# Optimization experiments

Measured on AMD Instinct MI355X. Metric: run time of the kernel, lower is better.

The kernel has to match this reference:

```python
import jax, jax.numpy as jnp
import numpy as np

DIM = 512
HEADS = 8
DIM_HEAD = 64
HIDDEN = HEADS * DIM_HEAD
SCALE = DIM_HEAD ** -0.5


def rmsnorm_ch(x, g):
    # F.normalize over channel dim (axis=1), then * g * sqrt(C)
    # x: [b, c, l], g: [c]
    n = jnp.maximum(jnp.linalg.norm(x, axis=1, keepdims=True), 1e-12)
    c = x.shape[1]
    return (x / n) * g[None, :, None] * (c ** 0.5)


def setup_inputs() -> dict:
    key = jax.random.key(0)
    ks = jax.random.split(key, 6)
    b, l = 8, 4096
    x = jax.random.normal(ks[0], (b, DIM, l), dtype=jnp.float32)
    g_in = jnp.ones((DIM,), dtype=jnp.float32)
    # conv1d kernel_size=1 == matmul; kaiming-ish init scale
    w_qkv = jax.random.normal(ks[1], (3 * HIDDEN, DIM), dtype=jnp.float32) * (1.0 / np.sqrt(DIM))
    w_out = jax.random.normal(ks[2], (DIM, HIDDEN), dtype=jnp.float32) * (1.0 / np.sqrt(HIDDEN))
    b_out = jax.random.normal(ks[3], (DIM,), dtype=jnp.float32) * 0.01
    g_out = jnp.ones((DIM,), dtype=jnp.float32)
    return {"x": x, "g_in": g_in, "w_qkv": w_qkv, "w_out": w_out, "b_out": b_out, "g_out": g_out}


def reference(x, g_in, w_qkv, w_out, b_out, g_out):
    b, c, l = x.shape
    residual = x
    xn = rmsnorm_ch(x, g_in)                       # [b, c, l]
    qkv = jnp.einsum('oc,bcl->bol', w_qkv, xn)     # [b, 3*hidden, l]
    q, k, v = jnp.split(qkv, 3, axis=1)            # each [b, hidden, l]
    def to_heads(t):
        return t.reshape(b, HEADS, DIM_HEAD, l)    # [b, h, d, l]
    q, k, v = to_heads(q), to_heads(k), to_heads(v)
    q = jax.nn.softmax(q, axis=2) * SCALE          # softmax over head-dim d
    k = jax.nn.softmax(k, axis=3)                  # softmax over sequence l
    context = jnp.einsum('bhdn,bhen->bhde', k, v)  # [b, h, d, e]
    out = jnp.einsum('bhde,bhdn->bhen', context, q)  # [b, h, e, l]
    out = out.reshape(b, HIDDEN, l)
    o = jnp.einsum('ch,bhl->bcl', w_out, out) + b_out[None, :, None]
    o = rmsnorm_ch(o, g_out)
    return o + residual
```

## Files before the change

### kernel.cpp

```cpp
#include <hip/hip_runtime.h>


#define BB 8
#define CC 512
#define LL 4096
#define HH 8
#define DH 64
#define TC 1536

__device__ __constant__ const float SQRT_C = 22.62741699796952f;
#define SCALE_Q 0.125f

typedef unsigned short bfr_t;
typedef __attribute__((ext_vector_type(8))) short short8;
typedef __attribute__((ext_vector_type(4))) float f32x4;

__device__ __forceinline__ float bf2f(bfr_t v) {
  union { unsigned u; float f; } c; c.u = ((unsigned)v) << 16; return c.f;
}
__device__ __forceinline__ bfr_t f2bf(float f) {
  union { float f; unsigned u; } c; c.f = f;
  unsigned u = c.u + 0x7fffu + ((c.u >> 16) & 1u);
  return (bfr_t)(u >> 16);
}

__device__ __forceinline__ void load_lds16(const bfr_t* g, short* l) {
  __builtin_amdgcn_global_load_lds(
      (const __attribute__((address_space(1))) void*)g,
      (__attribute__((address_space(3))) void*)l, 16, 0, 0);
}

__global__ __launch_bounds__(256) void conv_bf16(const float* __restrict__ in,
                                                 bfr_t* __restrict__ out, int n) {
  int i = blockIdx.x * 256 + threadIdx.x;
  if (i < n) out[i] = f2bf(in[i]);
}

__global__ __launch_bounds__(256) void fused_norm_transpose(
    const float* __restrict__ x, const float* __restrict__ g,
    bfr_t* __restrict__ xt) {
  __shared__ float tile[64][65];
  __shared__ float red[4][64];
  __shared__ float invn_s[64];
  int b = blockIdx.y, l0 = blockIdx.x * 64;
  int t = threadIdx.x, ll = t & 63, cg = t >> 6;
  const float* xb = x + (size_t)b * CC * LL + l0;
  float vals[8][16];
  float ss = 0.f;
#pragma unroll
  for (int ch = 0; ch < 8; ++ch) {
    int c0 = ch * 64;
#pragma unroll
    for (int i = 0; i < 16; ++i) {
      int c = i * 4 + cg;
      float v = xb[(size_t)(c0 + c) * LL + ll];
      vals[ch][i] = v;
      ss += v * v;
    }
  }
  red[cg][ll] = ss;
  __syncthreads();
  if (cg == 0) {
    float s = red[0][ll] + red[1][ll] + red[2][ll] + red[3][ll];
    invn_s[ll] = SQRT_C / fmaxf(sqrtf(s), 1e-12f);
  }
  __syncthreads();
  int lw = t >> 2, ccw = (t & 3) * 16;
  float iv = invn_s[lw];
#pragma unroll
  for (int ch = 0; ch < 8; ++ch) {
    int c0 = ch * 64;
#pragma unroll
    for (int i = 0; i < 16; ++i) tile[i * 4 + cg][ll] = vals[ch][i];
    __syncthreads();
    union { short s[16]; f32x4 v[2]; } pk;
#pragma unroll
    for (int u = 0; u < 16; ++u) {
      int c = ccw + u;
      pk.s[u] = (short)f2bf(tile[c][lw] * g[c0 + c] * iv);
    }
    bfr_t* dst = xt + ((size_t)b * LL + l0 + lw) * CC + c0 + ccw;
    *(f32x4*)dst = pk.v[0];
    *(f32x4*)(dst + 8) = pk.v[1];
    __syncthreads();
  }
}

__global__ __launch_bounds__(256) void gemm_bf16(
    const bfr_t* __restrict__ A, const bfr_t* __restrict__ Bt,
    bfr_t* __restrict__ Cout, const float* __restrict__ bias, int M) {
  const int K = 512;
  __shared__ short As[128 * 64];
  __shared__ short Bs[128 * 64];
  int b = blockIdx.z;
  int m0 = blockIdx.y * 128, n0 = blockIdx.x * 128;
  int t = threadIdx.x, lane = t & 63, wid = t >> 6;
  int wm = wid & 1, wn = wid >> 1;
  int quad = lane >> 4, r = lane & 15, r7 = r & 7;
  const bfr_t* Bbase = Bt + (size_t)b * LL * K;

  int lrow = lane >> 3;
  int lgran = (lane & 7) ^ lrow;
  const bfr_t* gA[4];
  const bfr_t* gB[4];
  short* lA[4];
  short* lB[4];
#pragma unroll
  for (int u = 0; u < 4; ++u) {
    int ch = wid * 4 + u;
    int row = ch * 8 + lrow;
    gA[u] = A + (size_t)(m0 + row) * K + lgran * 8;
    gB[u] = Bbase + (size_t)(n0 + row) * K + lgran * 8;
    lA[u] = As + ch * 512;
    lB[u] = Bs + ch * 512;
  }

  f32x4 acc[4][4] = {};

  for (int k0 = 0; k0 < K; k0 += 64) {
    __syncthreads();
#pragma unroll
    for (int u = 0; u < 4; ++u) {
      load_lds16(gA[u] + k0, lA[u]);
      load_lds16(gB[u] + k0, lB[u]);
    }
    __syncthreads();
#pragma unroll
    for (int ks = 0; ks < 2; ++ks) {
      short8 af[4], bfr8[4];
#pragma unroll
      for (int i = 0; i < 4; ++i) {
        int ga = ((ks * 4 + quad) ^ r7) * 8;
        af[i]   = *(const short8*)&As[(wm * 64 + i * 16 + r) * 64 + ga];
        bfr8[i] = *(const short8*)&Bs[(wn * 64 + i * 16 + r) * 64 + ga];
      }
#pragma unroll
      for (int i = 0; i < 4; ++i)
#pragma unroll
        for (int j = 0; j < 4; ++j)
          acc[i][j] = __builtin_amdgcn_mfma_f32_16x16x32_bf16(af[i], bfr8[j],
                                                              acc[i][j], 0, 0, 0);
    }
  }

  bfr_t* Cb = Cout + (size_t)b * M * LL;
#pragma unroll
  for (int i = 0; i < 4; ++i) {
#pragma unroll
    for (int reg = 0; reg < 4; ++reg) {
      int row = m0 + wm * 64 + i * 16 + quad * 4 + reg;
      float bi = bias ? bias[row] : 0.f;
#pragma unroll
      for (int j = 0; j < 4; ++j) {
        int col = n0 + wn * 64 + j * 16 + r;
        Cb[(size_t)row * LL + col] = f2bf(acc[i][j][reg] + bi);
      }
    }
  }
}

__global__ __launch_bounds__(256) void kstats(const bfr_t* __restrict__ qkv,
                                              float* __restrict__ kmax,
                                              float* __restrict__ ksum) {
  __shared__ float red[256];
  int row = blockIdx.x;
  int b = row >> 9, hd = row & 511;
  const bfr_t* kr = qkv + ((size_t)b * TC + 512 + hd) * LL;
  int t = threadIdx.x;
  float vals[16];
  float m = -1e30f;
#pragma unroll
  for (int i = 0; i < 16; ++i) {
    float v = bf2f(kr[t + i * 256]);
    vals[i] = v;
    m = fmaxf(m, v);
  }
  red[t] = m;
  __syncthreads();
  for (int s = 128; s > 0; s >>= 1) {
    if (t < s) red[t] = fmaxf(red[t], red[t + s]);
    __syncthreads();
  }
  m = red[0];
  __syncthreads();
  float ss = 0.f;
#pragma unroll
  for (int i = 0; i < 16; ++i) ss += __expf(vals[i] - m);
  red[t] = ss;
  __syncthreads();
  for (int s = 128; s > 0; s >>= 1) {
    if (t < s) red[t] += red[t + s];
    __syncthreads();
  }
  if (t == 0) { kmax[row] = m; ksum[row] = red[0]; }
}

__global__ __launch_bounds__(256) void context_mfma(
    const bfr_t* __restrict__ qkv, const float* __restrict__ kmax,
    float* __restrict__ ctx_p) {
  __shared__ float red[4][4096];
  int s = blockIdx.x, bh = blockIdx.y;
  int b = bh >> 3, h = bh & 7;
  int t = threadIdx.x, lane = t & 63, wid = t >> 6;
  int quad = lane >> 4, r = lane & 15;
  const bfr_t* kb = qkv + ((size_t)b * TC + 512 + h * 64) * LL;
  const bfr_t* vb = qkv + ((size_t)b * TC + 1024 + h * 64) * LL;
  float km[4];
#pragma unroll
  for (int i = 0; i < 4; ++i) km[i] = kmax[b * 512 + h * 64 + i * 16 + r];
  int n_base = s * 512 + wid * 128;
  f32x4 acc[4][4] = {};
#pragma unroll
  for (int ks = 0; ks < 4; ++ks) {
    int n0 = n_base + ks * 32;
    short8 af[4], bf8[4];
#pragma unroll
    for (int i = 0; i < 4; ++i) {
      union { short s[8]; short8 v8; } uk;
      uk.v8 = *(const short8*)&kb[(size_t)(i * 16 + r) * LL + n0 + quad * 8];
#pragma unroll
      for (int jj = 0; jj < 8; ++jj)
        uk.s[jj] = (short)f2bf(__expf(bf2f((bfr_t)uk.s[jj]) - km[i]));
      af[i] = uk.v8;
      bf8[i] = *(const short8*)&vb[(size_t)(i * 16 + r) * LL + n0 + quad * 8];
    }
#pragma unroll
    for (int i = 0; i < 4; ++i)
#pragma unroll
      for (int j = 0; j < 4; ++j)
        acc[i][j] = __builtin_amdgcn_mfma_f32_16x16x32_bf16(af[i], bf8[j],
                                                            acc[i][j], 0, 0, 0);
  }
#pragma unroll
  for (int i = 0; i < 4; ++i)
#pragma unroll
    for (int j = 0; j < 4; ++j)
#pragma unroll
      for (int reg = 0; reg < 4; ++reg)
        red[wid][(i * 16 + quad * 4 + reg) * 64 + j * 16 + r] = acc[i][j][reg];
  __syncthreads();
  float* out = ctx_p + ((size_t)bh * 8 + s) * 4096;
#pragma unroll
  for (int u = 0; u < 16; ++u) {
    int idx = u * 256 + t;
    out[idx] = red[0][idx] + red[1][idx] + red[2][idx] + red[3][idx];
  }
}

__global__ __launch_bounds__(256) void context_reduce(
    const float* __restrict__ ctx_p, const float* __restrict__ ksum,
    bfr_t* __restrict__ ctx_bf) {
  int bh = blockIdx.x;
  int b = bh >> 3, h = bh & 7;
  int t = threadIdx.x;
#pragma unroll
  for (int i = 0; i < 16; ++i) {
    int idx = i * 256 + t;
    int d = idx >> 6;
    float sum = 0.f;
#pragma unroll
    for (int s = 0; s < 8; ++s) sum += ctx_p[((size_t)bh * 8 + s) * 4096 + idx];
    ctx_bf[(size_t)bh * 4096 + idx] = f2bf(sum / ksum[b * 512 + h * 64 + d]);
  }
}

__global__ __launch_bounds__(256) void apply_fused(
    const bfr_t* __restrict__ qkv, const bfr_t* __restrict__ ctx_bf,
    bfr_t* __restrict__ out_t) {
  int b = blockIdx.z, h = blockIdx.y;
  int t = threadIdx.x, lane = t & 63, wid = t >> 6;
  int quad = lane >> 4, r = lane & 15;
  int n0 = blockIdx.x * 256 + wid * 64;
  const bfr_t* qb = qkv + ((size_t)b * TC + h * 64) * LL;
  const bfr_t* cb = ctx_bf + (size_t)(b * HH + h) * 4096;
  float v[4][16];
  float pm[4];
#pragma unroll
  for (int i = 0; i < 4; ++i) {
    pm[i] = -1e30f;
#pragma unroll
    for (int ks = 0; ks < 2; ++ks)
#pragma unroll
      for (int jj = 0; jj < 8; ++jj) {
        float q = bf2f(qb[(size_t)(ks * 32 + quad * 8 + jj) * LL + n0 + i * 16 + r]);
        v[i][ks * 8 + jj] = q;
        pm[i] = fmaxf(pm[i], q);
      }
  }
#pragma unroll
  for (int i = 0; i < 4; ++i) {
    pm[i] = fmaxf(pm[i], __shfl_xor(pm[i], 16, 64));
    pm[i] = fmaxf(pm[i], __shfl_xor(pm[i], 32, 64));
  }
  float psum[4];
#pragma unroll
  for (int i = 0; i < 4; ++i) {
    float s = 0.f;
#pragma unroll
    for (int u = 0; u < 16; ++u) { v[i][u] = __expf(v[i][u] - pm[i]); s += v[i][u]; }
    psum[i] = s;
  }
#pragma unroll
  for (int i = 0; i < 4; ++i) {
    psum[i] += __shfl_xor(psum[i], 16, 64);
    psum[i] += __shfl_xor(psum[i], 32, 64);
  }
  short8 af[2][4];
#pragma unroll
  for (int i = 0; i < 4; ++i) {
    float sc = SCALE_Q / psum[i];
#pragma unroll
    for (int ks = 0; ks < 2; ++ks) {
      union { short s[8]; short8 v8; } u;
#pragma unroll
      for (int jj = 0; jj < 8; ++jj) u.s[jj] = (short)f2bf(v[i][ks * 8 + jj] * sc);
      af[ks][i] = u.v8;
    }
  }
  short8 bfrag[2][4];
#pragma unroll
  for (int ks = 0; ks < 2; ++ks)
#pragma unroll
    for (int j = 0; j < 4; ++j) {
      union { short s[8]; short8 v8; } u;
#pragma unroll
      for (int jj = 0; jj < 8; ++jj)
        u.s[jj] = (short)cb[(ks * 32 + quad * 8 + jj) * 64 + j * 16 + r];
      bfrag[ks][j] = u.v8;
    }
  f32x4 acc[4][4] = {};
#pragma unroll
  for (int ks = 0; ks < 2; ++ks)
#pragma unroll
    for (int i = 0; i < 4; ++i)
#pragma unroll
      for (int j = 0; j < 4; ++j)
        acc[i][j] = __builtin_amdgcn_mfma_f32_16x16x32_bf16(af[ks][i], bfrag[ks][j],
                                                            acc[i][j], 0, 0, 0);
  bfr_t* dst = out_t + (size_t)b * LL * 512 + h * 64;
#pragma unroll
  for (int i = 0; i < 4; ++i)
#pragma unroll
    for (int reg = 0; reg < 4; ++reg) {
      int row = n0 + i * 16 + quad * 4 + reg;
#pragma unroll
      for (int j = 0; j < 4; ++j)
        dst[(size_t)row * 512 + j * 16 + r] = f2bf(acc[i][j][reg]);
    }
}

__global__ __launch_bounds__(256) void final_norm_res(
    const bfr_t* __restrict__ o, const float* __restrict__ g,
    const float* __restrict__ x, float* __restrict__ out) {
  __shared__ float red[4][64];
  __shared__ float invn[64];
  int b = blockIdx.y, l0 = blockIdx.x * 64;
  int t = threadIdx.x, ll = t & 63, cg = t >> 6;
  const bfr_t* ob = o + (size_t)b * CC * LL + l0 + ll;
  float ss = 0.f;
  for (int c = cg * 128; c < cg * 128 + 128; ++c) {
    float v = bf2f(ob[(size_t)c * LL]);
    ss += v * v;
  }
  red[cg][ll] = ss;
  __syncthreads();
  if (cg == 0) {
    float s = red[0][ll] + red[1][ll] + red[2][ll] + red[3][ll];
    invn[ll] = SQRT_C / fmaxf(sqrtf(s), 1e-12f);
  }
  __syncthreads();
  float iv = invn[ll];
  const float* xb = x + (size_t)b * CC * LL + l0 + ll;
  float* outb = out + (size_t)b * CC * LL + l0 + ll;
  for (int c = cg * 128; c < cg * 128 + 128; ++c) {
    float v = bf2f(ob[(size_t)c * LL]);
    outb[(size_t)c * LL] = v * g[c] * iv + xb[(size_t)c * LL];
  }
}

extern "C" void kernel_launch(void* const* d_in, const int* in_sizes, int n_in,
                              void* d_out, int out_size, void* d_ws,
                              size_t ws_size, hipStream_t stream) {
  const float* x     = (const float*)d_in[0];
  const float* g_in  = (const float*)d_in[1];
  const float* w_qkv = (const float*)d_in[2];
  const float* w_out = (const float*)d_in[3];
  const float* b_out = (const float*)d_in[4];
  const float* g_out = (const float*)d_in[5];
  float* out = (float*)d_out;

  char* ws = (char*)d_ws;
  const size_t off_wqkv  = 0;
  const size_t off_wout  = 1572864;
  const size_t off_kmax  = 2097152;
  const size_t off_ksum  = 2244608;
  const size_t off_ctx   = 2260992;
  const size_t off_ctxp  = 3309568;
  const size_t off_xt    = 11698176;
  const size_t off_qkv   = 45252608;
  const size_t ws_need   = 145915904;
  if (ws_size < ws_need) return;

  bfr_t* wqkv_bf = (bfr_t*)(ws + off_wqkv);
  bfr_t* wout_bf = (bfr_t*)(ws + off_wout);
  float* kmax    = (float*)(ws + off_kmax);
  float* ksum    = (float*)(ws + off_ksum);
  bfr_t* ctx_bf  = (bfr_t*)(ws + off_ctx);
  float* ctxp    = (float*)(ws + off_ctxp);
  bfr_t* xt      = (bfr_t*)(ws + off_xt);
  bfr_t* qkv     = (bfr_t*)(ws + off_qkv);
  bfr_t* o_bf    = (bfr_t*)(ws + off_qkv);

  conv_bf16<<<dim3((1536 * 512 + 255) / 256), 256, 0, stream>>>(w_qkv, wqkv_bf, 1536 * 512);
  conv_bf16<<<dim3((512 * 512 + 255) / 256), 256, 0, stream>>>(w_out, wout_bf, 512 * 512);
  fused_norm_transpose<<<dim3(LL / 64, BB), 256, 0, stream>>>(x, g_in, xt);
  gemm_bf16<<<dim3(LL / 128, TC / 128, BB), 256, 0, stream>>>(wqkv_bf, xt, qkv, nullptr, TC);
  kstats<<<dim3(BB * 512), 256, 0, stream>>>(qkv, kmax, ksum);
  context_mfma<<<dim3(8, BB * HH), 256, 0, stream>>>(qkv, kmax, ctxp);
  context_reduce<<<dim3(BB * HH), 256, 0, stream>>>(ctxp, ksum, ctx_bf);
  apply_fused<<<dim3(LL / 256, HH, BB), 256, 0, stream>>>(qkv, ctx_bf, xt);
  gemm_bf16<<<dim3(LL / 128, CC / 128, BB), 256, 0, stream>>>(wout_bf, xt, o_bf, b_out, CC);
  final_norm_res<<<dim3(LL / 64, BB), 256, 0, stream>>>(o_bf, g_out, x, out);
}
```

Before: 310.7 us.

## Switch GEMM to 32x32 MFMA, vectorize kstats loads, widen final norm, merge weight casts

The bf16 GEMM now uses 32x32x16 MFMA tiles with 2x2 accumulators per wave instead of 16x16x32 with 4x4, which cuts the number of LDS fragment reads and MFMA issues. kstats now reads each thread's 16 contiguous bf16 values with two 16-byte loads instead of strided scalar loads. final_norm_res runs 512 threads, caches its values in registers and reads the intermediate only once. The two weight conversion kernels are merged into a single launch. Risks are higher register pressure from the 64-value array in final_norm_res and a changed LDS bank pattern in the swizzled fragment reads.

```diff
diff --git a/kernel.cpp b/kernel.cpp
--- a/kernel.cpp
+++ b/kernel.cpp
@@ -14,6 +14,7 @@
 typedef unsigned short bfr_t;
 typedef __attribute__((ext_vector_type(8))) short short8;
 typedef __attribute__((ext_vector_type(4))) float f32x4;
+typedef __attribute__((ext_vector_type(16))) float f32x16;
 
 __device__ __forceinline__ float bf2f(bfr_t v) {
   union { unsigned u; float f; } c; c.u = ((unsigned)v) << 16; return c.f;
@@ -30,10 +31,13 @@
       (__attribute__((address_space(3))) void*)l, 16, 0, 0);
 }
 
-__global__ __launch_bounds__(256) void conv_bf16(const float* __restrict__ in,
-                                                 bfr_t* __restrict__ out, int n) {
+__global__ __launch_bounds__(256) void conv_bf16_2(
+    const float* __restrict__ in1, bfr_t* __restrict__ o1, int n1,
+    const float* __restrict__ in2, bfr_t* __restrict__ o2, int n2) {
   int i = blockIdx.x * 256 + threadIdx.x;
-  if (i < n) out[i] = f2bf(in[i]);
+  if (i < n1) o1[i] = f2bf(in1[i]);
+  int j = i - n1;
+  if (j >= 0 && j < n2) o2[j] = f2bf(in2[j]);
 }
 
 __global__ __launch_bounds__(256) void fused_norm_transpose(
@@ -96,7 +100,7 @@
   int m0 = blockIdx.y * 128, n0 = blockIdx.x * 128;
   int t = threadIdx.x, lane = t & 63, wid = t >> 6;
   int wm = wid & 1, wn = wid >> 1;
-  int quad = lane >> 4, r = lane & 15, r7 = r & 7;
+  int l31 = lane & 31, half = lane >> 5;
   const bfr_t* Bbase = Bt + (size_t)b * LL * K;
 
   int lrow = lane >> 3;
@@ -115,7 +119,7 @@
     lB[u] = Bs + ch * 512;
   }
 
-  f32x4 acc[4][4] = {};
+  f32x16 acc[2][2] = {};
 
   for (int k0 = 0; k0 < K; k0 += 64) {
     __syncthreads();
@@ -126,34 +130,40 @@
     }
     __syncthreads();
 #pragma unroll
-    for (int ks = 0; ks < 2; ++ks) {
-      short8 af[4], bfr8[4];
-#pragma unroll
-      for (int i = 0; i < 4; ++i) {
-        int ga = ((ks * 4 + quad) ^ r7) * 8;
-        af[i]   = *(const short8*)&As[(wm * 64 + i * 16 + r) * 64 + ga];
-        bfr8[i] = *(const short8*)&Bs[(wn * 64 + i * 16 + r) * 64 + ga];
+    for (int kk = 0; kk < 4; ++kk) {
+      short8 a[2], bq[2];
+#pragma unroll
+      for (int im = 0; im < 2; ++im) {
+        int row = wm * 64 + im * 32 + l31;
+        int gk = (kk * 2 + half) ^ (row & 7);
+        a[im] = *(const short8*)&As[row * 64 + gk * 8];
       }
 #pragma unroll
-      for (int i = 0; i < 4; ++i)
-#pragma unroll
-        for (int j = 0; j < 4; ++j)
-          acc[i][j] = __builtin_amdgcn_mfma_f32_16x16x32_bf16(af[i], bfr8[j],
-                                                              acc[i][j], 0, 0, 0);
+      for (int jn = 0; jn < 2; ++jn) {
+        int row = wn * 64 + jn * 32 + l31;
+        int gk = (kk * 2 + half) ^ (row & 7);
+        bq[jn] = *(const short8*)&Bs[row * 64 + gk * 8];
+      }
+#pragma unroll
+      for (int im = 0; im < 2; ++im)
+#pragma unroll
+        for (int jn = 0; jn < 2; ++jn)
+          acc[im][jn] = __builtin_amdgcn_mfma_f32_32x32x16_bf16(
+              a[im], bq[jn], acc[im][jn], 0, 0, 0);
     }
   }
 
   bfr_t* Cb = Cout + (size_t)b * M * LL;
 #pragma unroll
-  for (int i = 0; i < 4; ++i) {
-#pragma unroll
-    for (int reg = 0; reg < 4; ++reg) {
-      int row = m0 + wm * 64 + i * 16 + quad * 4 + reg;
+  for (int im = 0; im < 2; ++im) {
+#pragma unroll
+    for (int reg = 0; reg < 16; ++reg) {
+      int row = m0 + wm * 64 + im * 32 + (reg & 3) + 8 * (reg >> 2) + 4 * half;
       float bi = bias ? bias[row] : 0.f;
 #pragma unroll
-      for (int j = 0; j < 4; ++j) {
-        int col = n0 + wn * 64 + j * 16 + r;
-        Cb[(size_t)row * LL + col] = f2bf(acc[i][j][reg] + bi);
+      for (int jn = 0; jn < 2; ++jn) {
+        int col = n0 + wn * 64 + jn * 32 + l31;
+        Cb[(size_t)row * LL + col] = f2bf(acc[im][jn][reg] + bi);
       }
     }
   }
@@ -165,13 +175,16 @@
   __shared__ float red[256];
   int row = blockIdx.x;
   int b = row >> 9, hd = row & 511;
-  const bfr_t* kr = qkv + ((size_t)b * TC + 512 + hd) * LL;
+  const bfr_t* kr = qkv + ((size_t)b * TC + 512 + hd) * LL + (size_t)threadIdx.x * 16;
   int t = threadIdx.x;
+  union { short s[16]; short8 v[2]; } u;
+  u.v[0] = *(const short8*)kr;
+  u.v[1] = *(const short8*)(kr + 8);
   float vals[16];
   float m = -1e30f;
 #pragma unroll
   for (int i = 0; i < 16; ++i) {
-    float v = bf2f(kr[t + i * 256]);
+    float v = bf2f((bfr_t)u.s[i]);
     vals[i] = v;
     m = fmaxf(m, v);
   }
@@ -349,32 +362,39 @@
     }
 }
 
-__global__ __launch_bounds__(256) void final_norm_res(
+__global__ __launch_bounds__(512) void final_norm_res(
     const bfr_t* __restrict__ o, const float* __restrict__ g,
     const float* __restrict__ x, float* __restrict__ out) {
-  __shared__ float red[4][64];
+  __shared__ float red[8][64];
   __shared__ float invn[64];
   int b = blockIdx.y, l0 = blockIdx.x * 64;
   int t = threadIdx.x, ll = t & 63, cg = t >> 6;
   const bfr_t* ob = o + (size_t)b * CC * LL + l0 + ll;
+  float vals[64];
   float ss = 0.f;
-  for (int c = cg * 128; c < cg * 128 + 128; ++c) {
+#pragma unroll
+  for (int i = 0; i < 64; ++i) {
+    int c = cg * 64 + i;
     float v = bf2f(ob[(size_t)c * LL]);
+    vals[i] = v;
     ss += v * v;
   }
   red[cg][ll] = ss;
   __syncthreads();
   if (cg == 0) {
-    float s = red[0][ll] + red[1][ll] + red[2][ll] + red[3][ll];
+    float s = 0.f;
+#pragma unroll
+    for (int j = 0; j < 8; ++j) s += red[j][ll];
     invn[ll] = SQRT_C / fmaxf(sqrtf(s), 1e-12f);
   }
   __syncthreads();
   float iv = invn[ll];
   const float* xb = x + (size_t)b * CC * LL + l0 + ll;
   float* outb = out + (size_t)b * CC * LL + l0 + ll;
-  for (int c = cg * 128; c < cg * 128 + 128; ++c) {
-    float v = bf2f(ob[(size_t)c * LL]);
-    outb[(size_t)c * LL] = v * g[c] * iv + xb[(size_t)c * LL];
+#pragma unroll
+  for (int i = 0; i < 64; ++i) {
+    int c = cg * 64 + i;
+    outb[(size_t)c * LL] = vals[i] * g[c] * iv + xb[(size_t)c * LL];
   }
 }
 
@@ -411,8 +431,8 @@
   bfr_t* qkv     = (bfr_t*)(ws + off_qkv);
   bfr_t* o_bf    = (bfr_t*)(ws + off_qkv);
 
-  conv_bf16<<<dim3((1536 * 512 + 255) / 256), 256, 0, stream>>>(w_qkv, wqkv_bf, 1536 * 512);
-  conv_bf16<<<dim3((512 * 512 + 255) / 256), 256, 0, stream>>>(w_out, wout_bf, 512 * 512);
+  conv_bf16_2<<<dim3((1536 * 512 + 512 * 512 + 255) / 256), 256, 0, stream>>>(
+      w_qkv, wqkv_bf, 1536 * 512, w_out, wout_bf, 512 * 512);
   fused_norm_transpose<<<dim3(LL / 64, BB), 256, 0, stream>>>(x, g_in, xt);
   gemm_bf16<<<dim3(LL / 128, TC / 128, BB), 256, 0, stream>>>(wqkv_bf, xt, qkv, nullptr, TC);
   kstats<<<dim3(BB * 512), 256, 0, stream>>>(qkv, kmax, ksum);
@@ -420,5 +440,5 @@
   context_reduce<<<dim3(BB * HH), 256, 0, stream>>>(ctxp, ksum, ctx_bf);
   apply_fused<<<dim3(LL / 256, HH, BB), 256, 0, stream>>>(qkv, ctx_bf, xt);
   gemm_bf16<<<dim3(LL / 128, CC / 128, BB), 256, 0, stream>>>(wout_bf, xt, o_bf, b_out, CC);
-  final_norm_res<<<dim3(LL / 64, BB), 256, 0, stream>>>(o_bf, g_out, x, out);
-}
+  final_norm_res<<<dim3(LL / 64, BB), 512, 0, stream>>>(o_bf, g_out, x, out);
+}
```

Measured after the change: 310.1 us. Within noise of the previous version (-0.2%).
